# Optimization experiments

Measured on AMD Instinct MI355X. Metric: run time of the kernel, lower is better.

Reference implementation:

```python
import jax, jax.numpy as jnp
import numpy as np

DIM = 1024
HEADS = 16
DIM_HEAD = 64
INNER = HEADS * DIM_HEAD  # 1024


def xnorm(t, gamma):
    # t * gamma / ||t||_2 along last dim (keepdims)
    norm = jnp.linalg.norm(t, ord=2, axis=-1, keepdims=True)
    return t * gamma / norm


def setup_inputs() -> dict:
    key = jax.random.key(0)
    k0, k1, k2, k3, k4 = jax.random.split(key, 5)
    x = jax.random.normal(k0, (4, 4096, DIM), dtype=jnp.float32)
    # nn.Linear weights init with std=0.001, biases zero (per init_weights)
    W_qkv = jax.random.normal(k1, (DIM, 3 * INNER), dtype=jnp.float32) * 0.001
    W_o = jax.random.normal(k2, (INNER, DIM), dtype=jnp.float32) * 0.001
    b_o = jnp.zeros((DIM,), dtype=jnp.float32)
    gamma = jax.random.normal(k3, (1, HEADS, 1, 1), dtype=jnp.float32)
    return {"x": x, "W_qkv": W_qkv, "W_o": W_o, "b_o": b_o, "gamma": gamma}


def reference(x, W_qkv, W_o, b_o, gamma):
    b, n, _ = x.shape
    qkv = x @ W_qkv  # [b, n, 3*inner]
    q, k, v = jnp.split(qkv, 3, axis=-1)
    # [b, n, h*d] -> [b, h, n, d]
    reshape_heads = lambda t: t.reshape(b, n, HEADS, DIM_HEAD).transpose(0, 2, 1, 3)
    q, k, v = map(reshape_heads, (q, k, v))
    # kv = k^T v : [b, h, d, d]
    kv = jnp.einsum('bhnd,bhne->bhde', k, v)
    kv_n = xnorm(kv, gamma)
    q_n = xnorm(q, gamma)
    out = jnp.einsum('bhnd,bhde->bhne', q_n, kv_n)  # [b, h, n, d]
    out = out.transpose(0, 2, 1, 3).reshape(b, n, INNER)
    return out @ W_o + b_o
```

## Files before the change

kernel.cpp:

```cpp
#include <hip/hip_runtime.h>


typedef __bf16 bf16;
typedef bf16  bf16x8 __attribute__((ext_vector_type(8)));
typedef bf16  bf16x4 __attribute__((ext_vector_type(4)));
typedef float f32x4  __attribute__((ext_vector_type(4)));

#define BATCH   4
#define SEQ     4096
#define DIM     1024
#define HEADS   16
#define DHEAD   64
#define MTOK    (BATCH*SEQ)
#define N_QKV   (3*DIM)
#define NSPLIT  16

#define NB_PACK (MTOK*DIM/(8*256))
#define NB_T1   ((N_QKV/32)*(DIM/32))
#define NB_T2   ((DIM/32)*(DIM/32))

typedef __attribute__((address_space(1))) const void gas_v;
typedef __attribute__((address_space(3))) void las_v;

__device__ __forceinline__ void gld_lds16(const void* g, void* l) {
  __builtin_amdgcn_global_load_lds((gas_v*)g, (las_v*)l, 16, 0, 0);
}

__global__ __launch_bounds__(256) void prep(const float* __restrict__ x,
                                            const float* __restrict__ Wqkv,
                                            const float* __restrict__ Wo,
                                            bf16* __restrict__ xb,
                                            bf16* __restrict__ WqT,
                                            bf16* __restrict__ WoT) {
  const int bid = blockIdx.x;
  const int t   = threadIdx.x;
  if (bid < NB_PACK) {
    size_t i = (size_t)bid * 256 + t;
    f32x4 a = *(const f32x4*)&x[i * 8];
    f32x4 b = *(const f32x4*)&x[i * 8 + 4];
    bf16x8 o = {(bf16)a.x, (bf16)a.y, (bf16)a.z, (bf16)a.w,
                (bf16)b.x, (bf16)b.y, (bf16)b.z, (bf16)b.w};
    *(bf16x8*)&xb[i * 8] = o;
    return;
  }
  __shared__ float tile[32][33];
  const float* in; bf16* out; int R, C, bx, by;
  if (bid < NB_PACK + NB_T1) {
    int tid = bid - NB_PACK;
    in = Wqkv; out = WqT; R = DIM; C = N_QKV;
    bx = tid % (N_QKV / 32); by = tid / (N_QKV / 32);
  } else {
    int tid = bid - NB_PACK - NB_T1;
    in = Wo; out = WoT; R = DIM; C = DIM;
    bx = tid & 31; by = tid >> 5;
  }
  int c0 = bx * 32, r0 = by * 32;
  int tx = t & 31, ty = t >> 5;
#pragma unroll
  for (int i = 0; i < 32; i += 8)
    tile[ty + i][tx] = in[(size_t)(r0 + ty + i) * C + c0 + tx];
  __syncthreads();
#pragma unroll
  for (int i = 0; i < 32; i += 8)
    out[(size_t)(c0 + ty + i) * R + r0 + tx] = (bf16)tile[tx][ty + i];
}

template <int MODE>
__global__ __launch_bounds__(256) void gemm_bt(
    const bf16* __restrict__ A, const bf16* __restrict__ Bt, int N, int K,
    float* __restrict__ C, const float* __restrict__ bias,
    const float* __restrict__ gamma,
    bf16* __restrict__ qn, bf16* __restrict__ kb, bf16* __restrict__ vb) {
  __shared__ bf16 lA[128 * 32];
  __shared__ bf16 lB[128 * 32];
  const int t    = threadIdx.x;
  const int lane = t & 63;
  const int wv   = t >> 6;
  const int m0   = blockIdx.y * 128;
  const int n0   = blockIdx.x * 128;
  const int wm   = (wv >> 1) * 64;
  const int wn   = (wv & 1) * 64;
  const int lr   = lane & 15;
  const int ks   = lane >> 4;

  if (MODE == 2) Bt += (size_t)(m0 >> 12) * DIM * DIM;

  f32x4 acc[4][4];
#pragma unroll
  for (int i = 0; i < 4; i++)
#pragma unroll
    for (int j = 0; j < 4; j++) acc[i][j] = {0.f, 0.f, 0.f, 0.f};

  int aoff[4], boff[4];
#pragma unroll
  for (int i = 0; i < 4; i++) {
    int ra  = wm + i * 16 + lr;
    aoff[i] = ra * 32 + ((ks ^ ((ra >> 1) & 3)) * 8);
    int rb  = wn + i * 16 + lr;
    boff[i] = rb * 32 + ((ks ^ ((rb >> 1) & 3)) * 8);
  }
  const int srow = t >> 2;
  const int sseg = t & 3;

  for (int k0 = 0; k0 < K; k0 += 32) {
#pragma unroll
    for (int p = 0; p < 2; p++) {
      int row  = p * 64 + srow;
      int gseg = sseg ^ ((row >> 1) & 3);
      gld_lds16(A + (size_t)(m0 + row) * K + k0 + gseg * 8,
                &lA[row * 32 + sseg * 8]);
      gld_lds16(Bt + (size_t)(n0 + row) * K + k0 + gseg * 8,
                &lB[row * 32 + sseg * 8]);
    }
    __syncthreads();
    bf16x8 af[4], bfv[4];
#pragma unroll
    for (int i = 0; i < 4; i++) af[i] = *(const bf16x8*)&lA[aoff[i]];
#pragma unroll
    for (int j = 0; j < 4; j++) bfv[j] = *(const bf16x8*)&lB[boff[j]];
#pragma unroll
    for (int i = 0; i < 4; i++)
#pragma unroll
      for (int j = 0; j < 4; j++)
        acc[i][j] = __builtin_amdgcn_mfma_f32_16x16x32_bf16(af[i], bfv[j],
                                                            acc[i][j], 0, 0, 0);
    __syncthreads();
  }

  const int crow0 = m0 + wm + (lane >> 4) * 4;

  if (MODE == 2) {
    const int ccol0 = n0 + wn + lr;
#pragma unroll
    for (int i = 0; i < 4; i++)
#pragma unroll
      for (int j = 0; j < 4; j++) {
        int col = ccol0 + j * 16;
#pragma unroll
        for (int r = 0; r < 4; r++)
          C[(size_t)(crow0 + i * 16 + r) * N + col] = acc[i][j][r] + bias[col];
      }
  } else {
    const int seg = n0 >> 10;
    if (seg == 0) {
      const int h   = (n0 + wn) >> 6;
      const float g = gamma[h];
      const int col0 = n0 + wn + lr;
#pragma unroll
      for (int i = 0; i < 4; i++)
#pragma unroll
        for (int r = 0; r < 4; r++) {
          float p = acc[i][0][r] * acc[i][0][r] + acc[i][1][r] * acc[i][1][r]
                  + acc[i][2][r] * acc[i][2][r] + acc[i][3][r] * acc[i][3][r];
          p += __shfl_xor(p, 1);
          p += __shfl_xor(p, 2);
          p += __shfl_xor(p, 4);
          p += __shfl_xor(p, 8);
          float sc = g * rsqrtf(p);
          size_t rb = (size_t)(crow0 + i * 16 + r) * DIM + col0;
#pragma unroll
          for (int j = 0; j < 4; j++)
            qn[rb + j * 16] = (bf16)(acc[i][j][r] * sc);
        }
    } else {
      bf16* dst = (seg == 1) ? kb : vb;
      const int ccol0 = (n0 - seg * DIM) + wn + lr;
#pragma unroll
      for (int i = 0; i < 4; i++)
#pragma unroll
        for (int j = 0; j < 4; j++) {
          int col = ccol0 + j * 16;
#pragma unroll
          for (int r = 0; r < 4; r++)
            dst[(size_t)(crow0 + i * 16 + r) * DIM + col] = (bf16)acc[i][j][r];
        }
    }
  }
}

__global__ __launch_bounds__(256) void kv_partial(const bf16* __restrict__ kb,
                                                  const bf16* __restrict__ vb,
                                                  float* __restrict__ part) {
  __shared__ float lK[32 * 64];
  __shared__ float lV[32 * 64];
  const int t  = threadIdx.x;
  const int s  = blockIdx.x;
  const int bh = blockIdx.y;
  const int b  = bh >> 4, h = bh & 15;
  const size_t base = ((size_t)b * SEQ + s * (SEQ / NSPLIT)) * DIM + h * DHEAD;
  const int d0 = (t & 15) * 4, e0 = (t >> 4) * 4;
  const int rr = t >> 3, cc = (t & 7) * 8;

  float acc[4][4];
#pragma unroll
  for (int a = 0; a < 4; a++)
#pragma unroll
    for (int q = 0; q < 4; q++) acc[a][q] = 0.f;

  for (int nt = 0; nt < (SEQ / NSPLIT) / 32; nt++) {
    size_t g = base + (size_t)(nt * 32 + rr) * DIM + cc;
    bf16x8 k8 = *(const bf16x8*)(kb + g);
    bf16x8 v8 = *(const bf16x8*)(vb + g);
    f32x4 klo = {(float)k8[0], (float)k8[1], (float)k8[2], (float)k8[3]};
    f32x4 khi = {(float)k8[4], (float)k8[5], (float)k8[6], (float)k8[7]};
    f32x4 vlo = {(float)v8[0], (float)v8[1], (float)v8[2], (float)v8[3]};
    f32x4 vhi = {(float)v8[4], (float)v8[5], (float)v8[6], (float)v8[7]};
    *(f32x4*)&lK[rr * 64 + cc]     = klo;
    *(f32x4*)&lK[rr * 64 + cc + 4] = khi;
    *(f32x4*)&lV[rr * 64 + cc]     = vlo;
    *(f32x4*)&lV[rr * 64 + cc + 4] = vhi;
    __syncthreads();
#pragma unroll 8
    for (int nn = 0; nn < 32; nn++) {
      f32x4 kk = *(const f32x4*)&lK[nn * 64 + d0];
      f32x4 vv = *(const f32x4*)&lV[nn * 64 + e0];
#pragma unroll
      for (int a = 0; a < 4; a++)
#pragma unroll
        for (int q = 0; q < 4; q++) acc[a][q] += kk[a] * vv[q];
    }
    __syncthreads();
  }
  float* pb = part + ((size_t)bh * NSPLIT + s) * 4096;
#pragma unroll
  for (int a = 0; a < 4; a++) {
    f32x4 o = {acc[a][0], acc[a][1], acc[a][2], acc[a][3]};
    *(f32x4*)&pb[(d0 + a) * 64 + e0] = o;
  }
}

__global__ __launch_bounds__(256) void kv_norm(const float* __restrict__ part,
                                               const float* __restrict__ gamma,
                                               bf16* __restrict__ kvn) {
  const int t   = threadIdx.x;
  const int bh  = blockIdx.x >> 2;
  const int h   = bh & 15;
  const int d   = (blockIdx.x & 3) * 16 + (t >> 4);
  const int e0  = (t & 15) * 4;
  f32x4 v = {0.f, 0.f, 0.f, 0.f};
  for (int s = 0; s < NSPLIT; s++) {
    f32x4 a = *(const f32x4*)(part + ((size_t)bh * NSPLIT + s) * 4096 + d * 64 + e0);
    v.x += a.x; v.y += a.y; v.z += a.z; v.w += a.w;
  }
  float ss = v.x * v.x + v.y * v.y + v.z * v.z + v.w * v.w;
  ss += __shfl_xor(ss, 1);
  ss += __shfl_xor(ss, 2);
  ss += __shfl_xor(ss, 4);
  ss += __shfl_xor(ss, 8);
  float scale = gamma[h] * rsqrtf(ss);
  bf16x4 o = {(bf16)(v.x * scale), (bf16)(v.y * scale),
              (bf16)(v.z * scale), (bf16)(v.w * scale)};
  *(bf16x4*)&kvn[(size_t)bh * 4096 + d * 64 + e0] = o;
}

__global__ __launch_bounds__(256) void mfold(const bf16* __restrict__ WoT,
                                             const bf16* __restrict__ kvn,
                                             bf16* __restrict__ Mt) {
  __shared__ bf16 lA[128 * 64];
  __shared__ bf16 lB[64 * 64];
  const int t    = threadIdx.x;
  const int lane = t & 63;
  const int wv   = t >> 6;
  const int bh   = blockIdx.y;
  const int b    = bh >> 4, h = bh & 15;
  const int n0   = blockIdx.x * 128;

#pragma unroll
  for (int p = 0; p < 4; p++) {
    int c = p * 256 + t;
    int row = c >> 3, seg = c & 7;
    int gsk = seg ^ (row & 7);
    gld_lds16(WoT + (size_t)(n0 + row) * DIM + h * 64 + gsk * 8,
              &lA[row * 64 + seg * 8]);
  }
#pragma unroll
  for (int p = 0; p < 2; p++) {
    int c = p * 256 + t;
    int row = c >> 3, seg = c & 7;
    int gsk = seg ^ (row & 7);
    gld_lds16(kvn + (size_t)bh * 4096 + row * 64 + gsk * 8,
              &lB[row * 64 + seg * 8]);
  }
  __syncthreads();

  const int lr = lane & 15, ks = lane >> 4;
  f32x4 acc[2][4];
#pragma unroll
  for (int i = 0; i < 2; i++)
#pragma unroll
    for (int j = 0; j < 4; j++) acc[i][j] = {0.f, 0.f, 0.f, 0.f};

#pragma unroll
  for (int kk = 0; kk < 2; kk++) {
    bf16x8 af[2], bkv[4];
#pragma unroll
    for (int i = 0; i < 2; i++) {
      int row = wv * 32 + i * 16 + lr;
      int seg = (kk * 4 + ks) ^ (row & 7);
      af[i] = *(const bf16x8*)&lA[row * 64 + seg * 8];
    }
#pragma unroll
    for (int j = 0; j < 4; j++) {
      int row = j * 16 + lr;
      int seg = (kk * 4 + ks) ^ (row & 7);
      bkv[j] = *(const bf16x8*)&lB[row * 64 + seg * 8];
    }
#pragma unroll
    for (int i = 0; i < 2; i++)
#pragma unroll
      for (int j = 0; j < 4; j++)
        acc[i][j] = __builtin_amdgcn_mfma_f32_16x16x32_bf16(af[i], bkv[j],
                                                            acc[i][j], 0, 0, 0);
  }

  bf16* mb = Mt + (size_t)b * DIM * DIM;
#pragma unroll
  for (int i = 0; i < 2; i++)
#pragma unroll
    for (int j = 0; j < 4; j++) {
      int col = h * 64 + j * 16 + lr;
#pragma unroll
      for (int r = 0; r < 4; r++) {
        int row = n0 + wv * 32 + i * 16 + ks * 4 + r;
        mb[(size_t)row * DIM + col] = (bf16)acc[i][j][r];
      }
    }
}

extern "C" void kernel_launch(void* const* d_in, const int* in_sizes, int n_in,
                              void* d_out, int out_size, void* d_ws,
                              size_t ws_size, hipStream_t stream) {
  const float* x     = (const float*)d_in[0];
  const float* Wqkv  = (const float*)d_in[1];
  const float* Wo    = (const float*)d_in[2];
  const float* bo    = (const float*)d_in[3];
  const float* gamma = (const float*)d_in[4];
  float* out = (float*)d_out;

  char* ws = (char*)d_ws;
  size_t off = 0;
  bf16*  xb   = (bf16*)(ws + off);  off += (size_t)MTOK * DIM * 2;
  bf16*  WqT  = (bf16*)(ws + off);  off += (size_t)N_QKV * DIM * 2;
  bf16*  WoT  = (bf16*)(ws + off);  off += (size_t)DIM * DIM * 2;
  bf16*  kvn  = (bf16*)(ws + off);  off += (size_t)64 * 4096 * 2;
  bf16*  qn   = (bf16*)(ws + off);  off += (size_t)MTOK * DIM * 2;
  bf16*  kb   = (bf16*)(ws + off);  off += (size_t)MTOK * DIM * 2;
  bf16*  vb   = (bf16*)(ws + off);  off += (size_t)MTOK * DIM * 2;
  float* part = (float*)(ws + off); off += (size_t)64 * NSPLIT * 4096 * 4;
  bf16*  Mt   = (bf16*)(ws + off);  off += (size_t)BATCH * DIM * DIM * 2;

  prep<<<dim3(NB_PACK + NB_T1 + NB_T2), dim3(256), 0, stream>>>(
      x, Wqkv, Wo, xb, WqT, WoT);

  gemm_bt<1><<<dim3(N_QKV / 128, MTOK / 128), dim3(256), 0, stream>>>(
      xb, WqT, N_QKV, DIM, nullptr, nullptr, gamma, qn, kb, vb);

  kv_partial<<<dim3(NSPLIT, 64), dim3(256), 0, stream>>>(kb, vb, part);
  kv_norm<<<dim3(256), dim3(256), 0, stream>>>(part, gamma, kvn);

  mfold<<<dim3(DIM / 128, 64), dim3(256), 0, stream>>>(WoT, kvn, Mt);

  gemm_bt<2><<<dim3(DIM / 128, MTOK / 128), dim3(256), 0, stream>>>(
      qn, Mt, DIM, DIM, out, bo, nullptr, nullptr, nullptr, nullptr);
}
```

Measured before the change: 369.8 us.

## Replace 128x128 GEMM with 256x256 tile, 4-stage async LDS pipeline

Both bf16 GEMMs move from a 128x128 tile with 256 threads and a synchronous load/compute loop to a 256x256 tile with 512 threads. Global-to-LDS loads run through a 4-deep ring buffer, with explicit vmcnt waits, barriers and raised priority around the MFMA phases. This is meant to hide global load latency and double the reuse of each loaded tile. In exchange it uses 128KB of LDS per block and more accumulator registers, which limits occupancy, and the grid has fewer, larger blocks.

Result: faster. 312.8 us (-15.4%).

```diff
diff --git a/kernel.cpp b/kernel.cpp
--- a/kernel.cpp
+++ b/kernel.cpp
@@ -25,6 +25,19 @@
 __device__ __forceinline__ void gld_lds16(const void* g, void* l) {
   __builtin_amdgcn_global_load_lds((gas_v*)g, (las_v*)l, 16, 0, 0);
 }
+
+template <int VMN>
+__device__ __forceinline__ void vmwait() {
+  if constexpr (VMN == 8)      asm volatile("s_waitcnt vmcnt(8)" ::: "memory");
+  else if constexpr (VMN == 4) asm volatile("s_waitcnt vmcnt(4)" ::: "memory");
+  else if constexpr (VMN == 0) asm volatile("s_waitcnt vmcnt(0)" ::: "memory");
+}
+
+#define PH_BAR()                         \
+  do {                                   \
+    __builtin_amdgcn_s_barrier();        \
+    __builtin_amdgcn_sched_barrier(0);   \
+  } while (0)
 
 __global__ __launch_bounds__(256) void prep(const float* __restrict__ x,
                                             const float* __restrict__ Wqkv,
@@ -66,73 +79,110 @@
 }
 
 template <int MODE>
-__global__ __launch_bounds__(256) void gemm_bt(
+__global__ __launch_bounds__(512) void gemm256(
     const bf16* __restrict__ A, const bf16* __restrict__ Bt, int N, int K,
     float* __restrict__ C, const float* __restrict__ bias,
     const float* __restrict__ gamma,
     bf16* __restrict__ qn, bf16* __restrict__ kb, bf16* __restrict__ vb) {
-  __shared__ bf16 lA[128 * 32];
-  __shared__ bf16 lB[128 * 32];
+  __shared__ bf16 lds[4][2][256 * 32];
   const int t    = threadIdx.x;
   const int lane = t & 63;
   const int wv   = t >> 6;
-  const int m0   = blockIdx.y * 128;
-  const int n0   = blockIdx.x * 128;
-  const int wm   = (wv >> 1) * 64;
-  const int wn   = (wv & 1) * 64;
+  const int wr   = wv >> 2;
+  const int wc   = wv & 3;
+  const int m0   = blockIdx.y * 256;
+  const int n0   = blockIdx.x * 256;
   const int lr   = lane & 15;
   const int ks   = lane >> 4;
 
   if (MODE == 2) Bt += (size_t)(m0 >> 12) * DIM * DIM;
 
-  f32x4 acc[4][4];
-#pragma unroll
-  for (int i = 0; i < 4; i++)
-#pragma unroll
-    for (int j = 0; j < 4; j++) acc[i][j] = {0.f, 0.f, 0.f, 0.f};
-
-  int aoff[4], boff[4];
-#pragma unroll
-  for (int i = 0; i < 4; i++) {
-    int ra  = wm + i * 16 + lr;
+  int aoff[8], boff[4];
+#pragma unroll
+  for (int i = 0; i < 8; i++) {
+    int ra  = wr * 128 + i * 16 + lr;
     aoff[i] = ra * 32 + ((ks ^ ((ra >> 1) & 3)) * 8);
-    int rb  = wn + i * 16 + lr;
-    boff[i] = rb * 32 + ((ks ^ ((rb >> 1) & 3)) * 8);
-  }
+  }
+#pragma unroll
+  for (int j = 0; j < 4; j++) {
+    int rb  = wc * 64 + j * 16 + lr;
+    boff[j] = rb * 32 + ((ks ^ ((rb >> 1) & 3)) * 8);
+  }
+
   const int srow = t >> 2;
   const int sseg = t & 3;
 
-  for (int k0 = 0; k0 < K; k0 += 32) {
-#pragma unroll
-    for (int p = 0; p < 2; p++) {
-      int row  = p * 64 + srow;
+  const bf16* Asrc = A;
+  const bf16* Bsrc = Bt;
+  auto stage = [&](int half, int bufi, int tt) {
+    const bf16* src = half ? Bsrc : Asrc;
+    const int   rb0 = half ? n0 : m0;
+    const int   k0  = tt << 5;
+#pragma unroll
+    for (int p = 0; p < 2; ++p) {
+      int row  = p * 128 + srow;
       int gseg = sseg ^ ((row >> 1) & 3);
-      gld_lds16(A + (size_t)(m0 + row) * K + k0 + gseg * 8,
-                &lA[row * 32 + sseg * 8]);
-      gld_lds16(Bt + (size_t)(n0 + row) * K + k0 + gseg * 8,
-                &lB[row * 32 + sseg * 8]);
-    }
-    __syncthreads();
-    bf16x8 af[4], bfv[4];
-#pragma unroll
-    for (int i = 0; i < 4; i++) af[i] = *(const bf16x8*)&lA[aoff[i]];
-#pragma unroll
-    for (int j = 0; j < 4; j++) bfv[j] = *(const bf16x8*)&lB[boff[j]];
-#pragma unroll
-    for (int i = 0; i < 4; i++)
-#pragma unroll
-      for (int j = 0; j < 4; j++)
-        acc[i][j] = __builtin_amdgcn_mfma_f32_16x16x32_bf16(af[i], bfv[j],
-                                                            acc[i][j], 0, 0, 0);
-    __syncthreads();
-  }
-
-  const int crow0 = m0 + wm + (lane >> 4) * 4;
+      gld_lds16(src + (size_t)(rb0 + row) * K + k0 + gseg * 8,
+                &lds[bufi][half][row * 32 + sseg * 8]);
+    }
+  };
+
+  f32x4 acc[8][4];
+#pragma unroll
+  for (int i = 0; i < 8; i++)
+#pragma unroll
+    for (int j = 0; j < 4; j++) acc[i][j] = {0.f, 0.f, 0.f, 0.f};
+
+#define TILE(BUFI, DOSTAGE, STT, VM)                                          \
+  {                                                                           \
+    const int bb = (BUFI);                                                    \
+    bf16x8 bfv[4], af[4];                                                     \
+    _Pragma("unroll") for (int j = 0; j < 4; j++)                             \
+        bfv[j] = *(const bf16x8*)&lds[bb][1][boff[j]];                        \
+    _Pragma("unroll") for (int i = 0; i < 4; i++)                             \
+        af[i] = *(const bf16x8*)&lds[bb][0][aoff[i]];                         \
+    if (DOSTAGE) stage(0, (STT) & 3, (STT));                                  \
+    PH_BAR();                                                                 \
+    __builtin_amdgcn_s_setprio(1);                                            \
+    _Pragma("unroll") for (int i = 0; i < 4; i++)                             \
+        _Pragma("unroll") for (int j = 0; j < 4; j++)                         \
+            acc[i][j] = __builtin_amdgcn_mfma_f32_16x16x32_bf16(              \
+                af[i], bfv[j], acc[i][j], 0, 0, 0);                           \
+    __builtin_amdgcn_s_setprio(0);                                            \
+    PH_BAR();                                                                 \
+    _Pragma("unroll") for (int i = 0; i < 4; i++)                             \
+        af[i] = *(const bf16x8*)&lds[bb][0][aoff[4 + i]];                     \
+    if (DOSTAGE) stage(1, (STT) & 3, (STT));                                  \
+    vmwait<VM>();                                                             \
+    PH_BAR();                                                                 \
+    __builtin_amdgcn_s_setprio(1);                                            \
+    _Pragma("unroll") for (int i = 0; i < 4; i++)                             \
+        _Pragma("unroll") for (int j = 0; j < 4; j++)                         \
+            acc[4 + i][j] = __builtin_amdgcn_mfma_f32_16x16x32_bf16(          \
+                af[i], bfv[j], acc[4 + i][j], 0, 0, 0);                       \
+    __builtin_amdgcn_s_setprio(0);                                            \
+    PH_BAR();                                                                 \
+  }
+
+  const int NT = K >> 5;
+  stage(0, 0, 0); stage(1, 0, 0);
+  stage(0, 1, 1); stage(1, 1, 1);
+  stage(0, 2, 2); stage(1, 2, 2);
+  asm volatile("s_waitcnt vmcnt(8)" ::: "memory");
+  PH_BAR();
+
+  for (int tt = 0; tt < NT - 3; ++tt) TILE(tt & 3, true, tt + 3, 8);
+  TILE((NT - 3) & 3, false, 0, 4);
+  TILE((NT - 2) & 3, false, 0, 0);
+  TILE((NT - 1) & 3, false, 0, -1);
+#undef TILE
+
+  const int crow0 = m0 + wr * 128 + (lane >> 4) * 4;
 
   if (MODE == 2) {
-    const int ccol0 = n0 + wn + lr;
-#pragma unroll
-    for (int i = 0; i < 4; i++)
+    const int ccol0 = n0 + wc * 64 + lr;
+#pragma unroll
+    for (int i = 0; i < 8; i++)
 #pragma unroll
       for (int j = 0; j < 4; j++) {
         int col = ccol0 + j * 16;
@@ -143,11 +193,11 @@
   } else {
     const int seg = n0 >> 10;
     if (seg == 0) {
-      const int h   = (n0 + wn) >> 6;
-      const float g = gamma[h];
-      const int col0 = n0 + wn + lr;
-#pragma unroll
-      for (int i = 0; i < 4; i++)
+      const int h    = (n0 + wc * 64) >> 6;
+      const float g  = gamma[h];
+      const int col0 = n0 + wc * 64 + lr;
+#pragma unroll
+      for (int i = 0; i < 8; i++)
 #pragma unroll
         for (int r = 0; r < 4; r++) {
           float p = acc[i][0][r] * acc[i][0][r] + acc[i][1][r] * acc[i][1][r]
@@ -164,9 +214,9 @@
         }
     } else {
       bf16* dst = (seg == 1) ? kb : vb;
-      const int ccol0 = (n0 - seg * DIM) + wn + lr;
-#pragma unroll
-      for (int i = 0; i < 4; i++)
+      const int ccol0 = (n0 - (seg << 10)) + wc * 64 + lr;
+#pragma unroll
+      for (int i = 0; i < 8; i++)
 #pragma unroll
         for (int j = 0; j < 4; j++) {
           int col = ccol0 + j * 16;
@@ -352,7 +402,7 @@
   prep<<<dim3(NB_PACK + NB_T1 + NB_T2), dim3(256), 0, stream>>>(
       x, Wqkv, Wo, xb, WqT, WoT);
 
-  gemm_bt<1><<<dim3(N_QKV / 128, MTOK / 128), dim3(256), 0, stream>>>(
+  gemm256<1><<<dim3(N_QKV / 256, MTOK / 256), dim3(512), 0, stream>>>(
       xb, WqT, N_QKV, DIM, nullptr, nullptr, gamma, qn, kb, vb);
 
   kv_partial<<<dim3(NSPLIT, 64), dim3(256), 0, stream>>>(kb, vb, part);
@@ -360,6 +410,6 @@
 
   mfold<<<dim3(DIM / 128, 64), dim3(256), 0, stream>>>(WoT, kvn, Mt);
 
-  gemm_bt<2><<<dim3(DIM / 128, MTOK / 128), dim3(256), 0, stream>>>(
+  gemm256<2><<<dim3(DIM / 256, MTOK / 256), dim3(512), 0, stream>>>(
       qn, Mt, DIM, DIM, out, bo, nullptr, nullptr, nullptr, nullptr);
 }
```
